# Kernel tuning notes

Measured on AMD Instinct MI355X. Metric: run time of the kernel, lower is better.

Reference implementation:

```python
import jax, jax.numpy as jnp
import numpy as np

N = 100000  # nodes
E = 1600000  # edges
DIM_IN, DIM_H, DIM_OUT = 128, 64, 16


def gcn_conv(x, W, b, src, dst, n):
    """PyG GCNConv: symmetric-normalized aggregation with self-loops.
    out = D^{-1/2} (A + I) D^{-1/2} (x @ W) + b, degrees counted on dst.
    """
    h = x @ W  # [n, d_out]
    deg = jax.ops.segment_sum(jnp.ones((src.shape[0],), h.dtype), dst,
                              num_segments=n) + 1.0  # +1 for self-loop
    dinv = jax.lax.rsqrt(deg)  # [n]
    norm = dinv[src] * dinv[dst]  # [E]
    msg = h[src] * norm[:, None]  # [E, d_out] -- dominant memory traffic
    agg = jax.ops.segment_sum(msg, dst, num_segments=n)
    # self-loop contribution: norm_ii = dinv_i^2
    return agg + h * (dinv * dinv)[:, None] + b


def setup_inputs() -> dict:
    key = jax.random.key(0)
    k = jax.random.split(key, 6)
    x = jax.random.normal(k[0], (N, DIM_IN), dtype=jnp.float32)
    edge_index = jax.random.randint(k[1], (2, E), 0, N, dtype=jnp.int64)
    # Glorot-style init like torch Linear
    s1 = 1.0 / np.sqrt(DIM_IN)
    s2 = 1.0 / np.sqrt(DIM_H)
    W1 = jax.random.uniform(k[2], (DIM_IN, DIM_H), jnp.float32, -s1, s1)
    b1 = jnp.zeros((DIM_H,), jnp.float32)
    W2 = jax.random.uniform(k[3], (DIM_H, DIM_OUT), jnp.float32, -s2, s2)
    b2 = jnp.zeros((DIM_OUT,), jnp.float32)
    return {"x": x, "edge_index": edge_index, "W1": W1, "b1": b1,
            "W2": W2, "b2": b2}


def reference(x, edge_index, W1, b1, W2, b2):
    src, dst = edge_index[0], edge_index[1]
    n = x.shape[0]
    # dropout is identity in eval mode
    h = gcn_conv(x, W1, b1, src, dst, n)
    h = jax.nn.relu(h)
    h = gcn_conv(h, W2, b2, src, dst, n)
    return jax.nn.log_softmax(h, axis=1)
```

## Files before the change

kernel.cpp:

```cpp
#include <hip/hip_runtime.h>
#include <math.h>

#define DIM_IN 128
#define DIM_H 64
#define DIM_OUT 16
#define NBSHIFT 8
#define CHUNK 8192

typedef __attribute__((ext_vector_type(8))) short bf16x8;
typedef __attribute__((ext_vector_type(4))) float f32x4;

__device__ __forceinline__ ushort f2bf(float f) {
  uint u = __float_as_uint(f);
  return (ushort)((u + 0x7FFF + ((u >> 16) & 1)) >> 16);
}
__device__ __forceinline__ float bf2f(ushort s) {
  return __uint_as_float(((uint)s) << 16);
}
__device__ __forceinline__ uint cvtpk(float lo, float hi) {
  uint r;
  asm("v_cvt_pk_bf16_f32 %0, %1, %2" : "=v"(r) : "v"(lo), "v"(hi));
  return r;
}


__global__ __launch_bounds__(256) void k_hist1(const int* __restrict__ dst, int E,
                                               int* __restrict__ chunkhist) {
  __shared__ int lh[512];
  int t = threadIdx.x;
  int c = blockIdx.x;
  lh[t] = 0;
  lh[t + 256] = 0;
  __syncthreads();
  int e0 = c * CHUNK;
  int e1 = min(E, e0 + CHUNK);
  for (int i = e0 + t; i < e1; i += 256) atomicAdd(&lh[dst[i] >> NBSHIFT], 1);
  __syncthreads();
  chunkhist[c * 512 + t] = lh[t];
  chunkhist[c * 512 + t + 256] = lh[t + 256];
}

__global__ __launch_bounds__(256) void k_scanc(const int* __restrict__ chunkhist,
                                               int NC, int* __restrict__ cstart,
                                               int* __restrict__ gbhist) {
  __shared__ int sc[256];
  int t = threadIdx.x;
  int b = blockIdx.x;
  int v = (t < NC) ? chunkhist[t * 512 + b] : 0;
  sc[t] = v;
  __syncthreads();
  for (int off = 1; off < 256; off <<= 1) {
    int add = (t >= off) ? sc[t - off] : 0;
    __syncthreads();
    sc[t] += add;
    __syncthreads();
  }
  if (t < NC) cstart[t * 512 + b] = sc[t] - v;
  if (t == 255) gbhist[b] = sc[255];
}

__global__ __launch_bounds__(512) void k_bscan(const int* __restrict__ gbhist,
                                               int* __restrict__ bbase) {
  __shared__ int sb[512];
  int t = threadIdx.x;
  int v = gbhist[t];
  sb[t] = v;
  __syncthreads();
  for (int off = 1; off < 512; off <<= 1) {
    int add = (t >= off) ? sb[t - off] : 0;
    __syncthreads();
    sb[t] += add;
    __syncthreads();
  }
  bbase[t] = sb[t] - v;
}

__global__ __launch_bounds__(256) void k_part2(const int* __restrict__ src,
                                               const int* __restrict__ dst, int E,
                                               const int* __restrict__ cstart,
                                               const int* __restrict__ bbase,
                                               uint* __restrict__ pairs) {
  __shared__ int lcur[512];
  int t = threadIdx.x;
  int c = blockIdx.x;
  lcur[t] = cstart[c * 512 + t] + bbase[t];
  lcur[t + 256] = cstart[c * 512 + t + 256] + bbase[t + 256];
  __syncthreads();
  int e0 = c * CHUNK;
  int e1 = min(E, e0 + CHUNK);
  for (int i = e0 + t; i < e1; i += 256) {
    int d = dst[i];
    int pos = atomicAdd(&lcur[d >> NBSHIFT], 1);
    pairs[pos] = ((uint)src[i] << 8) | ((uint)d & 255u);
  }
}

__global__ __launch_bounds__(256) void k_csr(const uint* __restrict__ pairs,
                                             const int* __restrict__ gbhist,
                                             const int* __restrict__ bbase, int n,
                                             int* __restrict__ degi,
                                             float* __restrict__ dinv,
                                             int* __restrict__ rowptr,
                                             int* __restrict__ srcs) {
  __shared__ int nh[256];
  __shared__ int ncur[256];
  int t = threadIdx.x;
  int b = blockIdx.x;
  int base = bbase[b];
  int cnt = gbhist[b];
  nh[t] = 0;
  __syncthreads();
  for (int i = t; i < cnt; i += 256) atomicAdd(&nh[pairs[base + i] & 255u], 1);
  __syncthreads();
  int node = (b << NBSHIFT) + t;
  int v = nh[t];
  if (node < n) {
    degi[node] = v;
    dinv[node] = rsqrtf((float)v + 1.0f);
  }
  __syncthreads();
  for (int off = 1; off < 256; off <<= 1) {
    int add = (t >= off) ? nh[t - off] : 0;
    __syncthreads();
    nh[t] += add;
    __syncthreads();
  }
  int excl = nh[t] - v;
  if (node < n) rowptr[node] = base + excl;
  ncur[t] = base + excl;
  __syncthreads();
  for (int i = t; i < cnt; i += 256) {
    uint p = pairs[base + i];
    int pos = atomicAdd(&ncur[p & 255u], 1);
    srcs[pos] = (int)(p >> 8);
  }
}

__global__ __launch_bounds__(256) void k_wedge(const int* __restrict__ srcs,
                                               const float* __restrict__ dinv,
                                               ushort* __restrict__ wedge, int E) {
  int i = blockIdx.x * 256 + threadIdx.x;
  if (i < E) wedge[i] = f2bf(dinv[srcs[i]]);
}

__global__ __launch_bounds__(256, 4) void k_gemm1m(const float* __restrict__ x,
                                                   const float* __restrict__ W,
                                                   ushort* __restrict__ h, int n,
                                                   int nTiles) {
  const int t = threadIdx.x;
  const int lane = t & 63;
  const int wid = blockIdx.x * 4 + (t >> 6);
  const int nW = gridDim.x * 4;
  const int cc = lane & 15;
  const int kb = (lane >> 4) * 8;

  bf16x8 bfrag[4][4];
#pragma unroll
  for (int kc = 0; kc < 4; ++kc)
#pragma unroll
    for (int nt = 0; nt < 4; ++nt) {
      union { bf16x8 v; uint u[4]; } fb;
#pragma unroll
      for (int j = 0; j < 4; ++j) {
        float lo = W[(size_t)(kc * 32 + kb + 2 * j) * DIM_H + nt * 16 + cc];
        float hi = W[(size_t)(kc * 32 + kb + 2 * j + 1) * DIM_H + nt * 16 + cc];
        fb.u[j] = cvtpk(lo, hi);
      }
      bfrag[kc][nt] = fb.v;
    }

  for (int tile = wid; tile < nTiles; tile += nW) {
    int row0 = tile * 16;
    int ra = row0 + cc;
    if (ra > n - 1) ra = n - 1;
    const float* xp = x + (size_t)ra * DIM_IN;
    f32x4 acc[4] = {{0.f, 0.f, 0.f, 0.f},
                    {0.f, 0.f, 0.f, 0.f},
                    {0.f, 0.f, 0.f, 0.f},
                    {0.f, 0.f, 0.f, 0.f}};
#pragma unroll
    for (int kc = 0; kc < 4; ++kc) {
      float4 a0 = *(const float4*)(xp + kc * 32 + kb);
      float4 a1 = *(const float4*)(xp + kc * 32 + kb + 4);
      union { bf16x8 v; uint u[4]; } fa;
      fa.u[0] = cvtpk(a0.x, a0.y);
      fa.u[1] = cvtpk(a0.z, a0.w);
      fa.u[2] = cvtpk(a1.x, a1.y);
      fa.u[3] = cvtpk(a1.z, a1.w);
#pragma unroll
      for (int nt = 0; nt < 4; ++nt)
        acc[nt] = __builtin_amdgcn_mfma_f32_16x16x32_bf16(fa.v, bfrag[kc][nt],
                                                          acc[nt], 0, 0, 0);
    }
    int rbase = row0 + (lane >> 4) * 4;
#pragma unroll
    for (int nt = 0; nt < 4; ++nt) {
      int col = nt * 16 + cc;
#pragma unroll
      for (int j = 0; j < 4; ++j) {
        int r = rbase + j;
        if (r < n) h[(size_t)r * DIM_H + col] = f2bf(acc[nt][j]);
      }
    }
  }
}

__global__ __launch_bounds__(256) void k_gemm2(const ushort* __restrict__ a,
                                               const float* __restrict__ W,
                                               ushort* __restrict__ h2, int n) {
  __shared__ float Ws[64][16];
  const int t = threadIdx.x;
  for (int i = t; i < 64 * 16; i += 256) Ws[i >> 4][i & 15] = W[i];
  __syncthreads();
  int r = blockIdx.x * 256 + t;
  if (r >= n) return;
  const uint4* ap = (const uint4*)(a + (size_t)r * DIM_H);
  float acc[16] = {};
#pragma unroll
  for (int k8 = 0; k8 < 8; ++k8) {
    uint4 v = ap[k8];
    uint w[4] = {v.x, v.y, v.z, v.w};
#pragma unroll
    for (int p = 0; p < 4; ++p) {
      float v0 = fmaxf(bf2f((ushort)(w[p] & 0xffff)), 0.f);
      float v1 = fmaxf(bf2f((ushort)(w[p] >> 16)), 0.f);
      int k = k8 * 8 + p * 2;
#pragma unroll
      for (int j = 0; j < 16; ++j) acc[j] = fmaf(v0, Ws[k][j], acc[j]);
#pragma unroll
      for (int j = 0; j < 16; ++j) acc[j] = fmaf(v1, Ws[k + 1][j], acc[j]);
    }
  }
  ushort4* hp = (ushort4*)(h2 + (size_t)r * DIM_OUT);
#pragma unroll
  for (int q = 0; q < 4; ++q) {
    ushort4 o;
    o.x = f2bf(acc[q * 4 + 0]);
    o.y = f2bf(acc[q * 4 + 1]);
    o.z = f2bf(acc[q * 4 + 2]);
    o.w = f2bf(acc[q * 4 + 3]);
    hp[q] = o;
  }
}


__global__ __launch_bounds__(256) void k_gather64(const ushort* __restrict__ h,
                                                  const int* __restrict__ srcs,
                                                  const ushort* __restrict__ wedge,
                                                  const int* __restrict__ rowptr,
                                                  const int* __restrict__ deg,
                                                  const float* __restrict__ dinv,
                                                  const float* __restrict__ b,
                                                  ushort* __restrict__ out, int n) {
  int node = blockIdx.x * 4 + (threadIdx.x >> 6);
  int lane = threadIdx.x & 63;
  int g = lane >> 4;
  int q = lane & 15;
  if (node >= n) return;
  int start = rowptr[node];
  int cnt = deg[node];
  float dd = dinv[node];
  float a0 = 0.f, a1 = 0.f, a2 = 0.f, a3 = 0.f;
  for (int j0 = 0; j0 < cnt; j0 += 64) {
    int rem = cnt - j0;
    if (rem > 64) rem = 64;
    int s_l = (lane < rem) ? srcs[start + j0 + lane] : 0;
    float w_l = (lane < rem) ? bf2f(wedge[start + j0 + lane]) * dd : 0.0f;
    for (int j = 0; j < rem; j += 16) {
      int i0 = j + g, i1 = j + 4 + g, i2 = j + 8 + g, i3 = j + 12 + g;
      int s0 = __shfl(s_l, i0);
      float w0 = __shfl(w_l, i0);
      int s1 = __shfl(s_l, i1);
      float w1 = __shfl(w_l, i1);
      int s2 = __shfl(s_l, i2);
      float w2 = __shfl(w_l, i2);
      int s3 = __shfl(s_l, i3);
      float w3 = __shfl(w_l, i3);
      uint2 v0 = *(const uint2*)(h + (size_t)s0 * DIM_H + q * 4);
      uint2 v1 = *(const uint2*)(h + (size_t)s1 * DIM_H + q * 4);
      uint2 v2 = *(const uint2*)(h + (size_t)s2 * DIM_H + q * 4);
      uint2 v3 = *(const uint2*)(h + (size_t)s3 * DIM_H + q * 4);
      a0 = fmaf(bf2f((ushort)(v0.x & 0xffff)), w0, a0);
      a1 = fmaf(bf2f((ushort)(v0.x >> 16)), w0, a1);
      a2 = fmaf(bf2f((ushort)(v0.y & 0xffff)), w0, a2);
      a3 = fmaf(bf2f((ushort)(v0.y >> 16)), w0, a3);
      a0 = fmaf(bf2f((ushort)(v1.x & 0xffff)), w1, a0);
      a1 = fmaf(bf2f((ushort)(v1.x >> 16)), w1, a1);
      a2 = fmaf(bf2f((ushort)(v1.y & 0xffff)), w1, a2);
      a3 = fmaf(bf2f((ushort)(v1.y >> 16)), w1, a3);
      a0 = fmaf(bf2f((ushort)(v2.x & 0xffff)), w2, a0);
      a1 = fmaf(bf2f((ushort)(v2.x >> 16)), w2, a1);
      a2 = fmaf(bf2f((ushort)(v2.y & 0xffff)), w2, a2);
      a3 = fmaf(bf2f((ushort)(v2.y >> 16)), w2, a3);
      a0 = fmaf(bf2f((ushort)(v3.x & 0xffff)), w3, a0);
      a1 = fmaf(bf2f((ushort)(v3.x >> 16)), w3, a1);
      a2 = fmaf(bf2f((ushort)(v3.y & 0xffff)), w3, a2);
      a3 = fmaf(bf2f((ushort)(v3.y >> 16)), w3, a3);
    }
  }
  a0 += __shfl_xor(a0, 16); a0 += __shfl_xor(a0, 32);
  a1 += __shfl_xor(a1, 16); a1 += __shfl_xor(a1, 32);
  a2 += __shfl_xor(a2, 16); a2 += __shfl_xor(a2, 32);
  a3 += __shfl_xor(a3, 16); a3 += __shfl_xor(a3, 32);
  if (g == 0) {
    uint2 sv = *(const uint2*)(h + (size_t)node * DIM_H + q * 4);
    float s2 = dd * dd;
    a0 = fmaf(bf2f((ushort)(sv.x & 0xffff)), s2, a0) + b[4 * q + 0];
    a1 = fmaf(bf2f((ushort)(sv.x >> 16)), s2, a1) + b[4 * q + 1];
    a2 = fmaf(bf2f((ushort)(sv.y & 0xffff)), s2, a2) + b[4 * q + 2];
    a3 = fmaf(bf2f((ushort)(sv.y >> 16)), s2, a3) + b[4 * q + 3];
    uint lo = cvtpk(a0, a1);
    uint hi = cvtpk(a2, a3);
    *(uint2*)(out + (size_t)node * DIM_H + q * 4) = make_uint2(lo, hi);
  }
}

__global__ __launch_bounds__(256) void k_gather16(const ushort* __restrict__ h,
                                                  const int* __restrict__ srcs,
                                                  const ushort* __restrict__ wedge,
                                                  const int* __restrict__ rowptr,
                                                  const int* __restrict__ deg,
                                                  const float* __restrict__ dinv,
                                                  const float* __restrict__ b,
                                                  float* __restrict__ out, int n) {
  int node = blockIdx.x * 16 + (threadIdx.x >> 4);
  int lane = threadIdx.x & 63;
  int lane16 = lane & 15;
  int gbase = lane & 48;
  int e = (lane >> 2) & 3;
  int c = lane & 3;
  if (node >= n) return;
  int start = rowptr[node];
  int cnt = deg[node];
  float dd = dinv[node];
  const int iA = gbase + e, iB = gbase + 4 + e, iC = gbase + 8 + e,
            iD = gbase + 12 + e;
  float a0 = 0.f, a1 = 0.f, a2 = 0.f, a3 = 0.f;
  for (int j0 = 0; j0 < cnt; j0 += 16) {
    int rem = cnt - j0;
    if (rem > 16) rem = 16;
    int s_l = (lane16 < rem) ? srcs[start + j0 + lane16] : 0;
    float w_l = (lane16 < rem) ? bf2f(wedge[start + j0 + lane16]) * dd : 0.0f;
    int sA = __shfl(s_l, iA);
    float wA = __shfl(w_l, iA);
    int sB = __shfl(s_l, iB);
    float wB = __shfl(w_l, iB);
    int sC = __shfl(s_l, iC);
    float wC = __shfl(w_l, iC);
    int sD = __shfl(s_l, iD);
    float wD = __shfl(w_l, iD);
    uint2 vA = *(const uint2*)(h + (size_t)sA * DIM_OUT + c * 4);
    uint2 vB = *(const uint2*)(h + (size_t)sB * DIM_OUT + c * 4);
    uint2 vC = *(const uint2*)(h + (size_t)sC * DIM_OUT + c * 4);
    uint2 vD = *(const uint2*)(h + (size_t)sD * DIM_OUT + c * 4);
    a0 = fmaf(bf2f((ushort)(vA.x & 0xffff)), wA, a0);
    a1 = fmaf(bf2f((ushort)(vA.x >> 16)), wA, a1);
    a2 = fmaf(bf2f((ushort)(vA.y & 0xffff)), wA, a2);
    a3 = fmaf(bf2f((ushort)(vA.y >> 16)), wA, a3);
    a0 = fmaf(bf2f((ushort)(vB.x & 0xffff)), wB, a0);
    a1 = fmaf(bf2f((ushort)(vB.x >> 16)), wB, a1);
    a2 = fmaf(bf2f((ushort)(vB.y & 0xffff)), wB, a2);
    a3 = fmaf(bf2f((ushort)(vB.y >> 16)), wB, a3);
    a0 = fmaf(bf2f((ushort)(vC.x & 0xffff)), wC, a0);
    a1 = fmaf(bf2f((ushort)(vC.x >> 16)), wC, a1);
    a2 = fmaf(bf2f((ushort)(vC.y & 0xffff)), wC, a2);
    a3 = fmaf(bf2f((ushort)(vC.y >> 16)), wC, a3);
    a0 = fmaf(bf2f((ushort)(vD.x & 0xffff)), wD, a0);
    a1 = fmaf(bf2f((ushort)(vD.x >> 16)), wD, a1);
    a2 = fmaf(bf2f((ushort)(vD.y & 0xffff)), wD, a2);
    a3 = fmaf(bf2f((ushort)(vD.y >> 16)), wD, a3);
  }
  a0 += __shfl_xor(a0, 4); a0 += __shfl_xor(a0, 8);
  a1 += __shfl_xor(a1, 4); a1 += __shfl_xor(a1, 8);
  a2 += __shfl_xor(a2, 4); a2 += __shfl_xor(a2, 8);
  a3 += __shfl_xor(a3, 4); a3 += __shfl_xor(a3, 8);
  uint2 sv = *(const uint2*)(h + (size_t)node * DIM_OUT + c * 4);
  float s2 = dd * dd;
  a0 = fmaf(bf2f((ushort)(sv.x & 0xffff)), s2, a0) + b[4 * c + 0];
  a1 = fmaf(bf2f((ushort)(sv.x >> 16)), s2, a1) + b[4 * c + 1];
  a2 = fmaf(bf2f((ushort)(sv.y & 0xffff)), s2, a2) + b[4 * c + 2];
  a3 = fmaf(bf2f((ushort)(sv.y >> 16)), s2, a3) + b[4 * c + 3];
  float m = fmaxf(fmaxf(a0, a1), fmaxf(a2, a3));
  m = fmaxf(m, __shfl_xor(m, 1));
  m = fmaxf(m, __shfl_xor(m, 2));
  float ssum = expf(a0 - m) + expf(a1 - m) + expf(a2 - m) + expf(a3 - m);
  ssum += __shfl_xor(ssum, 1);
  ssum += __shfl_xor(ssum, 2);
  float l = m + logf(ssum);
  if (e == 0)
    *(float4*)(out + (size_t)node * DIM_OUT + c * 4) =
        make_float4(a0 - l, a1 - l, a2 - l, a3 - l);
}


extern "C" void kernel_launch(void* const* d_in, const int* in_sizes, int n_in,
                              void* d_out, int out_size, void* d_ws, size_t ws_size,
                              hipStream_t stream) {
  const float* x  = (const float*)d_in[0];
  const int*   ei = (const int*)d_in[1];
  const float* W1 = (const float*)d_in[2];
  const float* b1 = (const float*)d_in[3];
  const float* W2 = (const float*)d_in[4];
  const float* b2 = (const float*)d_in[5];
  float* out = (float*)d_out;

  const int n = in_sizes[0] / DIM_IN;
  const int E = in_sizes[1] / 2;
  const int* srcv = ei;
  const int* dstv = ei + E;
  const int NB = (n + 255) >> NBSHIFT;
  const int NC = (E + CHUNK - 1) / CHUNK;

  char* wsb = (char*)d_ws;
  int* degi      = (int*)wsb;   wsb += (size_t)n * 4;
  int* rowptr    = (int*)wsb;   wsb += (size_t)n * 4;
  float* dinv    = (float*)wsb; wsb += (size_t)n * 4;
  int* gbhist    = (int*)wsb;   wsb += 512 * 4;
  int* bbase     = (int*)wsb;   wsb += 512 * 4;
  int* chunkhist = (int*)wsb;   wsb += (size_t)256 * 512 * 4;
  int* cstart    = (int*)wsb;   wsb += (size_t)256 * 512 * 4;
  int* srcs      = (int*)wsb;   wsb += (size_t)E * 4;
  ushort* wedge  = (ushort*)wsb; wsb += (size_t)E * 2;
  ushort* h1     = (ushort*)wsb; wsb += (size_t)n * DIM_H * 2;
  ushort* agg1   = (ushort*)wsb; wsb += (size_t)n * DIM_H * 2;
  ushort* h2     = (ushort*)wsb; wsb += (size_t)n * DIM_OUT * 2;
  uint* pairs = (uint*)agg1;

  k_hist1<<<NC, 256, 0, stream>>>(dstv, E, chunkhist);
  k_scanc<<<512, 256, 0, stream>>>(chunkhist, NC, cstart, gbhist);
  k_bscan<<<1, 512, 0, stream>>>(gbhist, bbase);
  k_part2<<<NC, 256, 0, stream>>>(srcv, dstv, E, cstart, bbase, pairs);
  k_csr<<<NB, 256, 0, stream>>>(pairs, gbhist, bbase, n, degi, dinv, rowptr, srcs);
  k_wedge<<<(E + 255) / 256, 256, 0, stream>>>(srcs, dinv, wedge, E);

  k_gemm1m<<<512, 256, 0, stream>>>(x, W1, h1, n, (n + 15) / 16);
  k_gather64<<<(n + 3) / 4, 256, 0, stream>>>(h1, srcs, wedge, rowptr, degi, dinv,
                                              b1, agg1, n);

  k_gemm2<<<(n + 255) / 256, 256, 0, stream>>>(agg1, W2, h2, n);
  k_gather16<<<(n + 15) / 16, 256, 0, stream>>>(h2, srcs, wedge, rowptr, degi, dinv,
                                                b2, out, n);
}
```

Baseline: 148.5 us.

## Fuse CSR build into one cooperative kernel and pack edge weight with source

Replaces the six CSR-construction kernels with a single cooperative kernel that uses grid-wide syncs between the histogram, scan, partition and CSR phases. The separate edge-weight pass is dropped: each edge entry now packs a bf16 dinv value into the upper bits and the 17-bit source index into the lower bits, so the gathers read one word per edge instead of two arrays. The ReLU moves from the second GEMM's load into the first gather's epilogue. In exchange, the cooperative launch needs all NB blocks resident at once, and the 17-bit index limits the node count.

```diff
diff --git a/kernel.cpp b/kernel.cpp
--- a/kernel.cpp
+++ b/kernel.cpp
@@ -1,5 +1,8 @@
 #include <hip/hip_runtime.h>
+#include <hip/hip_cooperative_groups.h>
 #include <math.h>
+
+namespace cg = cooperative_groups;
 
 #define DIM_IN 128
 #define DIM_H 64
@@ -23,124 +26,117 @@
   return r;
 }
 
-
-__global__ __launch_bounds__(256) void k_hist1(const int* __restrict__ dst, int E,
-                                               int* __restrict__ chunkhist) {
+__global__ __launch_bounds__(256) void k_csrbuild(
+    const int* __restrict__ src, const int* __restrict__ dst, int E, int n,
+    int NC, int NB, int* __restrict__ chunkhist, int* __restrict__ cstart,
+    int* __restrict__ gbhist, int* __restrict__ bbase, uint* __restrict__ pairs,
+    int* __restrict__ degi, float* __restrict__ dinv, int* __restrict__ rowptr,
+    uint* __restrict__ esrc) {
+  cg::grid_group grid = cg::this_grid();
   __shared__ int lh[512];
-  int t = threadIdx.x;
-  int c = blockIdx.x;
-  lh[t] = 0;
-  lh[t + 256] = 0;
-  __syncthreads();
-  int e0 = c * CHUNK;
-  int e1 = min(E, e0 + CHUNK);
-  for (int i = e0 + t; i < e1; i += 256) atomicAdd(&lh[dst[i] >> NBSHIFT], 1);
-  __syncthreads();
-  chunkhist[c * 512 + t] = lh[t];
-  chunkhist[c * 512 + t + 256] = lh[t + 256];
-}
-
-__global__ __launch_bounds__(256) void k_scanc(const int* __restrict__ chunkhist,
-                                               int NC, int* __restrict__ cstart,
-                                               int* __restrict__ gbhist) {
-  __shared__ int sc[256];
-  int t = threadIdx.x;
-  int b = blockIdx.x;
-  int v = (t < NC) ? chunkhist[t * 512 + b] : 0;
-  sc[t] = v;
-  __syncthreads();
-  for (int off = 1; off < 256; off <<= 1) {
-    int add = (t >= off) ? sc[t - off] : 0;
-    __syncthreads();
-    sc[t] += add;
-    __syncthreads();
-  }
-  if (t < NC) cstart[t * 512 + b] = sc[t] - v;
-  if (t == 255) gbhist[b] = sc[255];
-}
-
-__global__ __launch_bounds__(512) void k_bscan(const int* __restrict__ gbhist,
-                                               int* __restrict__ bbase) {
-  __shared__ int sb[512];
-  int t = threadIdx.x;
-  int v = gbhist[t];
-  sb[t] = v;
-  __syncthreads();
-  for (int off = 1; off < 512; off <<= 1) {
-    int add = (t >= off) ? sb[t - off] : 0;
-    __syncthreads();
-    sb[t] += add;
-    __syncthreads();
-  }
-  bbase[t] = sb[t] - v;
-}
-
-__global__ __launch_bounds__(256) void k_part2(const int* __restrict__ src,
-                                               const int* __restrict__ dst, int E,
-                                               const int* __restrict__ cstart,
-                                               const int* __restrict__ bbase,
-                                               uint* __restrict__ pairs) {
-  __shared__ int lcur[512];
-  int t = threadIdx.x;
-  int c = blockIdx.x;
-  lcur[t] = cstart[c * 512 + t] + bbase[t];
-  lcur[t + 256] = cstart[c * 512 + t + 256] + bbase[t + 256];
-  __syncthreads();
-  int e0 = c * CHUNK;
-  int e1 = min(E, e0 + CHUNK);
-  for (int i = e0 + t; i < e1; i += 256) {
-    int d = dst[i];
-    int pos = atomicAdd(&lcur[d >> NBSHIFT], 1);
-    pairs[pos] = ((uint)src[i] << 8) | ((uint)d & 255u);
-  }
-}
-
-__global__ __launch_bounds__(256) void k_csr(const uint* __restrict__ pairs,
-                                             const int* __restrict__ gbhist,
-                                             const int* __restrict__ bbase, int n,
-                                             int* __restrict__ degi,
-                                             float* __restrict__ dinv,
-                                             int* __restrict__ rowptr,
-                                             int* __restrict__ srcs) {
   __shared__ int nh[256];
   __shared__ int ncur[256];
-  int t = threadIdx.x;
-  int b = blockIdx.x;
-  int base = bbase[b];
-  int cnt = gbhist[b];
-  nh[t] = 0;
-  __syncthreads();
-  for (int i = t; i < cnt; i += 256) atomicAdd(&nh[pairs[base + i] & 255u], 1);
-  __syncthreads();
-  int node = (b << NBSHIFT) + t;
-  int v = nh[t];
-  if (node < n) {
-    degi[node] = v;
-    dinv[node] = rsqrtf((float)v + 1.0f);
-  }
-  __syncthreads();
-  for (int off = 1; off < 256; off <<= 1) {
-    int add = (t >= off) ? nh[t - off] : 0;
-    __syncthreads();
-    nh[t] += add;
-    __syncthreads();
-  }
-  int excl = nh[t] - v;
-  if (node < n) rowptr[node] = base + excl;
-  ncur[t] = base + excl;
-  __syncthreads();
-  for (int i = t; i < cnt; i += 256) {
-    uint p = pairs[base + i];
-    int pos = atomicAdd(&ncur[p & 255u], 1);
-    srcs[pos] = (int)(p >> 8);
-  }
-}
-
-__global__ __launch_bounds__(256) void k_wedge(const int* __restrict__ srcs,
-                                               const float* __restrict__ dinv,
-                                               ushort* __restrict__ wedge, int E) {
-  int i = blockIdx.x * 256 + threadIdx.x;
-  if (i < E) wedge[i] = f2bf(dinv[srcs[i]]);
+  const int t = threadIdx.x;
+  const int bid = blockIdx.x;
+  const int nblk = gridDim.x;
+
+  for (int c = bid; c < NC; c += nblk) {
+    lh[t] = 0;
+    lh[t + 256] = 0;
+    __syncthreads();
+    int e0 = c * CHUNK, e1 = min(E, e0 + CHUNK);
+    for (int i = e0 + t; i < e1; i += 256) atomicAdd(&lh[dst[i] >> NBSHIFT], 1);
+    __syncthreads();
+    chunkhist[c * 512 + t] = lh[t];
+    chunkhist[c * 512 + t + 256] = lh[t + 256];
+    __syncthreads();
+  }
+  grid.sync();
+
+  for (int b = bid; b < 512; b += nblk) {
+    int v = (t < NC) ? chunkhist[t * 512 + b] : 0;
+    lh[t] = v;
+    __syncthreads();
+    for (int off = 1; off < 256; off <<= 1) {
+      int add = (t >= off) ? lh[t - off] : 0;
+      __syncthreads();
+      lh[t] += add;
+      __syncthreads();
+    }
+    if (t < NC) cstart[t * 512 + b] = lh[t] - v;
+    if (t == 255) gbhist[b] = lh[255];
+    __syncthreads();
+  }
+  grid.sync();
+
+  if (bid == 0) {
+    int v0 = gbhist[t], v1 = gbhist[t + 256];
+    lh[t] = v0;
+    lh[t + 256] = v1;
+    __syncthreads();
+    for (int off = 1; off < 256; off <<= 1) {
+      int a0 = (t >= off) ? lh[t - off] : 0;
+      int a1 = (t >= off) ? lh[256 + t - off] : 0;
+      __syncthreads();
+      lh[t] += a0;
+      lh[256 + t] += a1;
+      __syncthreads();
+    }
+    int tot0 = lh[255];
+    bbase[t] = lh[t] - v0;
+    bbase[t + 256] = lh[256 + t] - v1 + tot0;
+  }
+  grid.sync();
+
+  for (int c = bid; c < NC; c += nblk) {
+    lh[t] = cstart[c * 512 + t] + bbase[t];
+    lh[t + 256] = cstart[c * 512 + t + 256] + bbase[t + 256];
+    __syncthreads();
+    int e0 = c * CHUNK, e1 = min(E, e0 + CHUNK);
+    for (int i = e0 + t; i < e1; i += 256) {
+      int d = dst[i];
+      int pos = atomicAdd(&lh[d >> NBSHIFT], 1);
+      pairs[pos] = ((uint)src[i] << 8) | ((uint)d & 255u);
+    }
+    __syncthreads();
+  }
+  grid.sync();
+
+  int base = 0, cnt = 0;
+  if (bid < NB) {
+    base = bbase[bid];
+    cnt = gbhist[bid];
+    nh[t] = 0;
+    __syncthreads();
+    for (int i = t; i < cnt; i += 256) atomicAdd(&nh[pairs[base + i] & 255u], 1);
+    __syncthreads();
+    int node = (bid << NBSHIFT) + t;
+    int v = nh[t];
+    if (node < n) {
+      degi[node] = v;
+      dinv[node] = rsqrtf((float)v + 1.0f);
+    }
+    __syncthreads();
+    for (int off = 1; off < 256; off <<= 1) {
+      int add = (t >= off) ? nh[t - off] : 0;
+      __syncthreads();
+      nh[t] += add;
+      __syncthreads();
+    }
+    int excl = nh[t] - v;
+    if (node < n) rowptr[node] = base + excl;
+    ncur[t] = base + excl;
+  }
+  grid.sync();
+
+  if (bid < NB) {
+    for (int i = t; i < cnt; i += 256) {
+      uint p = pairs[base + i];
+      int pos = atomicAdd(&ncur[p & 255u], 1);
+      uint s = p >> 8;
+      esrc[pos] = ((uint)f2bf(dinv[s]) << 17) | s;
+    }
+  }
 }
 
 __global__ __launch_bounds__(256, 4) void k_gemm1m(const float* __restrict__ x,
@@ -222,8 +218,8 @@
     uint w[4] = {v.x, v.y, v.z, v.w};
 #pragma unroll
     for (int p = 0; p < 4; ++p) {
-      float v0 = fmaxf(bf2f((ushort)(w[p] & 0xffff)), 0.f);
-      float v1 = fmaxf(bf2f((ushort)(w[p] >> 16)), 0.f);
+      float v0 = bf2f((ushort)(w[p] & 0xffff));
+      float v1 = bf2f((ushort)(w[p] >> 16));
       int k = k8 * 8 + p * 2;
 #pragma unroll
       for (int j = 0; j < 16; ++j) acc[j] = fmaf(v0, Ws[k][j], acc[j]);
@@ -245,8 +241,7 @@
 
 
 __global__ __launch_bounds__(256) void k_gather64(const ushort* __restrict__ h,
-                                                  const int* __restrict__ srcs,
-                                                  const ushort* __restrict__ wedge,
+                                                  const uint* __restrict__ esrc,
                                                   const int* __restrict__ rowptr,
                                                   const int* __restrict__ deg,
                                                   const float* __restrict__ dinv,
@@ -264,8 +259,9 @@
   for (int j0 = 0; j0 < cnt; j0 += 64) {
     int rem = cnt - j0;
     if (rem > 64) rem = 64;
-    int s_l = (lane < rem) ? srcs[start + j0 + lane] : 0;
-    float w_l = (lane < rem) ? bf2f(wedge[start + j0 + lane]) * dd : 0.0f;
+    uint p_l = (lane < rem) ? esrc[start + j0 + lane] : 0u;
+    int s_l = (int)(p_l & 0x1FFFFu);
+    float w_l = bf2f((ushort)(p_l >> 17)) * dd;
     for (int j = 0; j < rem; j += 16) {
       int i0 = j + g, i1 = j + 4 + g, i2 = j + 8 + g, i3 = j + 12 + g;
       int s0 = __shfl(s_l, i0);
@@ -305,10 +301,10 @@
   if (g == 0) {
     uint2 sv = *(const uint2*)(h + (size_t)node * DIM_H + q * 4);
     float s2 = dd * dd;
-    a0 = fmaf(bf2f((ushort)(sv.x & 0xffff)), s2, a0) + b[4 * q + 0];
-    a1 = fmaf(bf2f((ushort)(sv.x >> 16)), s2, a1) + b[4 * q + 1];
-    a2 = fmaf(bf2f((ushort)(sv.y & 0xffff)), s2, a2) + b[4 * q + 2];
-    a3 = fmaf(bf2f((ushort)(sv.y >> 16)), s2, a3) + b[4 * q + 3];
+    a0 = fmaxf(fmaf(bf2f((ushort)(sv.x & 0xffff)), s2, a0) + b[4 * q + 0], 0.f);
+    a1 = fmaxf(fmaf(bf2f((ushort)(sv.x >> 16)), s2, a1) + b[4 * q + 1], 0.f);
+    a2 = fmaxf(fmaf(bf2f((ushort)(sv.y & 0xffff)), s2, a2) + b[4 * q + 2], 0.f);
+    a3 = fmaxf(fmaf(bf2f((ushort)(sv.y >> 16)), s2, a3) + b[4 * q + 3], 0.f);
     uint lo = cvtpk(a0, a1);
     uint hi = cvtpk(a2, a3);
     *(uint2*)(out + (size_t)node * DIM_H + q * 4) = make_uint2(lo, hi);
@@ -316,8 +312,7 @@
 }
 
 __global__ __launch_bounds__(256) void k_gather16(const ushort* __restrict__ h,
-                                                  const int* __restrict__ srcs,
-                                                  const ushort* __restrict__ wedge,
+                                                  const uint* __restrict__ esrc,
                                                   const int* __restrict__ rowptr,
                                                   const int* __restrict__ deg,
                                                   const float* __restrict__ dinv,
@@ -339,8 +334,9 @@
   for (int j0 = 0; j0 < cnt; j0 += 16) {
     int rem = cnt - j0;
     if (rem > 16) rem = 16;
-    int s_l = (lane16 < rem) ? srcs[start + j0 + lane16] : 0;
-    float w_l = (lane16 < rem) ? bf2f(wedge[start + j0 + lane16]) * dd : 0.0f;
+    uint p_l = (lane16 < rem) ? esrc[start + j0 + lane16] : 0u;
+    int s_l = (int)(p_l & 0x1FFFFu);
+    float w_l = bf2f((ushort)(p_l >> 17)) * dd;
     int sA = __shfl(s_l, iA);
     float wA = __shfl(w_l, iA);
     int sB = __shfl(s_l, iB);
@@ -404,12 +400,12 @@
   const float* b2 = (const float*)d_in[5];
   float* out = (float*)d_out;
 
-  const int n = in_sizes[0] / DIM_IN;
-  const int E = in_sizes[1] / 2;
+  int n = in_sizes[0] / DIM_IN;
+  int E = in_sizes[1] / 2;
   const int* srcv = ei;
   const int* dstv = ei + E;
-  const int NB = (n + 255) >> NBSHIFT;
-  const int NC = (E + CHUNK - 1) / CHUNK;
+  int NB = (n + 255) >> NBSHIFT;
+  int NC = (E + CHUNK - 1) / CHUNK;
 
   char* wsb = (char*)d_ws;
   int* degi      = (int*)wsb;   wsb += (size_t)n * 4;
@@ -419,25 +415,27 @@
   int* bbase     = (int*)wsb;   wsb += 512 * 4;
   int* chunkhist = (int*)wsb;   wsb += (size_t)256 * 512 * 4;
   int* cstart    = (int*)wsb;   wsb += (size_t)256 * 512 * 4;
-  int* srcs      = (int*)wsb;   wsb += (size_t)E * 4;
-  ushort* wedge  = (ushort*)wsb; wsb += (size_t)E * 2;
+  uint* esrc     = (uint*)wsb;  wsb += (size_t)E * 4;
   ushort* h1     = (ushort*)wsb; wsb += (size_t)n * DIM_H * 2;
   ushort* agg1   = (ushort*)wsb; wsb += (size_t)n * DIM_H * 2;
   ushort* h2     = (ushort*)wsb; wsb += (size_t)n * DIM_OUT * 2;
   uint* pairs = (uint*)agg1;
 
-  k_hist1<<<NC, 256, 0, stream>>>(dstv, E, chunkhist);
-  k_scanc<<<512, 256, 0, stream>>>(chunkhist, NC, cstart, gbhist);
-  k_bscan<<<1, 512, 0, stream>>>(gbhist, bbase);
-  k_part2<<<NC, 256, 0, stream>>>(srcv, dstv, E, cstart, bbase, pairs);
-  k_csr<<<NB, 256, 0, stream>>>(pairs, gbhist, bbase, n, degi, dinv, rowptr, srcs);
-  k_wedge<<<(E + 255) / 256, 256, 0, stream>>>(srcs, dinv, wedge, E);
+  {
+    void* args[] = {(void*)&srcv, (void*)&dstv, (void*)&E, (void*)&n,
+                    (void*)&NC,  (void*)&NB,   (void*)&chunkhist,
+                    (void*)&cstart, (void*)&gbhist, (void*)&bbase,
+                    (void*)&pairs, (void*)&degi, (void*)&dinv,
+                    (void*)&rowptr, (void*)&esrc};
+    hipLaunchCooperativeKernel((void*)k_csrbuild, dim3(NB), dim3(256), args, 0,
+                               stream);
+  }
 
   k_gemm1m<<<512, 256, 0, stream>>>(x, W1, h1, n, (n + 15) / 16);
-  k_gather64<<<(n + 3) / 4, 256, 0, stream>>>(h1, srcs, wedge, rowptr, degi, dinv,
-                                              b1, agg1, n);
+  k_gather64<<<(n + 3) / 4, 256, 0, stream>>>(h1, esrc, rowptr, degi, dinv, b1,
+                                              agg1, n);
 
   k_gemm2<<<(n + 255) / 256, 256, 0, stream>>>(agg1, W2, h2, n);
-  k_gather16<<<(n + 15) / 16, 256, 0, stream>>>(h2, srcs, wedge, rowptr, degi, dinv,
-                                                b2, out, n);
-}
+  k_gather16<<<(n + 15) / 16, 256, 0, stream>>>(h2, esrc, rowptr, degi, dinv, b2,
+                                                out, n);
+}
```

New measurement: 364.7 us. 146% more time.
